# Kernel optimization log

Hardware: AMD Instinct MI355X
Metric: run time of the kernel (lower is better)

## Reference

```python
import math
import jax, jax.numpy as jnp
import numpy as np

B, N, D, H = 2, 2048, 1024, 16

def setup_inputs() -> dict:
    key = jax.random.key(0)
    ks = jax.random.split(key, 5)
    x = jax.random.normal(ks[0], (B, N, D), dtype=jnp.float32)
    # causal mask: True = masked (matches masked_fill semantics)
    mask = jnp.broadcast_to(jnp.triu(jnp.ones((N, N), dtype=bool), k=1), (B, N, N))
    sc = 0.02
    Wqkv = jax.random.normal(ks[1], (3 * D, D), dtype=jnp.float32) * sc
    bqkv = jax.random.normal(ks[2], (3 * D,), dtype=jnp.float32) * sc
    Wo = jax.random.normal(ks[3], (D, D), dtype=jnp.float32) * sc
    bo = jax.random.normal(ks[4], (D,), dtype=jnp.float32) * sc
    return {"x": x, "mask": mask, "Wqkv": Wqkv, "bqkv": bqkv, "Wo": Wo, "bo": bo}

def reference(x, mask, Wqkv, bqkv, Wo, bo):
    b, n, d = x.shape
    h = H
    s = d // h
    qkv = x @ Wqkv.T + bqkv                       # [b, n, 3d]
    q, k, v = jnp.split(qkv, 3, axis=2)           # each [b, n, d]
    def heads(z):
        return z.reshape(b, n, h, s).transpose(0, 2, 1, 3)  # [b, h, n, s]
    q, k, v = heads(q), heads(k), heads(v)
    q = q / jnp.asarray(math.sqrt(s), q.dtype)
    a = jnp.einsum('bhqs,bhks->bhqk', q, k)       # [b, h, n, n]
    a = jnp.where(mask[:, None, :, :], -jnp.inf, a)
    a = jax.nn.softmax(a, axis=-1)
    y = jnp.einsum('bhqk,bhks->bhqs', a, v)       # [b, h, n, s]
    y = y.transpose(0, 2, 1, 3).reshape(b, n, d)
    return y @ Wo.T + bo
```

## Files before the change

### kernel.cpp

```cpp
#include <hip/hip_runtime.h>
#include <hip/hip_bf16.h>
#include <stdint.h>

#define BB 2
#define NN 2048
#define DD 1024
#define HH 16
#define SS 64

typedef short short8 __attribute__((ext_vector_type(8)));
typedef float f32x4 __attribute__((ext_vector_type(4)));

__device__ __forceinline__ float bf2f(uint16_t u) {
    return __uint_as_float(((uint32_t)u) << 16);
}
__device__ __forceinline__ uint16_t f2bf(float f) {
    uint32_t u = __float_as_uint(f);
    return (uint16_t)((u + 0x7FFFu + ((u >> 16) & 1u)) >> 16);
}
__device__ __forceinline__ short8 cvt8(float4 a, float4 b) {
    short8 s;
    s[0] = (short)f2bf(a.x); s[1] = (short)f2bf(a.y);
    s[2] = (short)f2bf(a.z); s[3] = (short)f2bf(a.w);
    s[4] = (short)f2bf(b.x); s[5] = (short)f2bf(b.y);
    s[6] = (short)f2bf(b.z); s[7] = (short)f2bf(b.w);
    return s;
}

__device__ __forceinline__ void load_lds16(const uint16_t* g, uint16_t* l) {
    __builtin_amdgcn_global_load_lds(
        (const __attribute__((address_space(1))) void*)g,
        (__attribute__((address_space(3))) void*)l, 16, 0, 0);
}

#define XE  (4096 * 1024)
#define WQE (3072 * 1024)
#define WOE (1024 * 1024)

__global__ __launch_bounds__(256) void cvt_all(
    const float* __restrict__ x, const float* __restrict__ wq,
    const float* __restrict__ wo, uint16_t* __restrict__ dst)
{
    int i = (blockIdx.x * 256 + threadIdx.x) * 8;
    const float* src;
    int off;
    if (i < XE)            { src = x;  off = i; }
    else if (i < XE + WQE) { src = wq; off = i - XE; }
    else                   { src = wo; off = i - XE - WQE; }
    float4 a = *(const float4*)(src + off);
    float4 b = *(const float4*)(src + off + 4);
    *(short8*)(dst + i) = cvt8(a, b);
}

__global__ __launch_bounds__(256) void gemm_qkv(
    const uint16_t* __restrict__ X, const uint16_t* __restrict__ W,
    const float* __restrict__ bias,
    uint16_t* __restrict__ Qb, uint16_t* __restrict__ Kb, uint16_t* __restrict__ Vt)
{
    __shared__ __align__(16) uint16_t smem[18432];
    uint16_t* As0 = smem;
    uint16_t* As1 = smem + 4096;
    uint16_t* Bs0 = smem + 8192;
    uint16_t* Bs1 = smem + 12288;

    const int tid = threadIdx.x;
    const int w = tid >> 6, l = tid & 63;
    const int lq = l & 15, lg = l >> 4;
    const int wm = w >> 1, wn = w & 1;

    const int flat = blockIdx.x + blockIdx.y * 24;
    const int xcd = flat & 7, g = flat >> 3;
    const int n0 = (xcd * 3 + (g % 3)) * 128;
    const int m0 = (g / 3) * 128;

    f32x4 acc[4][4] = {};

    for (int k0 = 0; k0 < 1024; k0 += 64) {
        __syncthreads();
        #pragma unroll
        for (int j = 0; j < 2; ++j) {
            const int c = (j * 4 + w) * 64 + l;
            const size_t ra = (size_t)(m0 + (c >> 2)) * 1024 + k0 + (c & 3) * 8;
            const size_t rb = (size_t)(n0 + (c >> 2)) * 1024 + k0 + (c & 3) * 8;
            load_lds16(X + ra,      As0 + (j * 4 + w) * 512);
            load_lds16(X + ra + 32, As1 + (j * 4 + w) * 512);
            load_lds16(W + rb,      Bs0 + (j * 4 + w) * 512);
            load_lds16(W + rb + 32, Bs1 + (j * 4 + w) * 512);
        }
        __syncthreads();
        short8 af[4], bfr[4];
        #pragma unroll
        for (int mi = 0; mi < 4; ++mi)
            af[mi] = *(const short8*)&As0[(wm * 64 + mi * 16 + lq) * 32 + lg * 8];
        #pragma unroll
        for (int ni = 0; ni < 4; ++ni)
            bfr[ni] = *(const short8*)&Bs0[(wn * 64 + ni * 16 + lq) * 32 + lg * 8];
        #pragma unroll
        for (int mi = 0; mi < 4; ++mi)
            #pragma unroll
            for (int ni = 0; ni < 4; ++ni)
                acc[mi][ni] = __builtin_amdgcn_mfma_f32_16x16x32_bf16(
                    af[mi], bfr[ni], acc[mi][ni], 0, 0, 0);
        #pragma unroll
        for (int mi = 0; mi < 4; ++mi)
            af[mi] = *(const short8*)&As1[(wm * 64 + mi * 16 + lq) * 32 + lg * 8];
        #pragma unroll
        for (int ni = 0; ni < 4; ++ni)
            bfr[ni] = *(const short8*)&Bs1[(wn * 64 + ni * 16 + lq) * 32 + lg * 8];
        #pragma unroll
        for (int mi = 0; mi < 4; ++mi)
            #pragma unroll
            for (int ni = 0; ni < 4; ++ni)
                acc[mi][ni] = __builtin_amdgcn_mfma_f32_16x16x32_bf16(
                    af[mi], bfr[ni], acc[mi][ni], 0, 0, 0);
    }

    __syncthreads();
    const int part = n0 >> 10;
    const int hh = ((n0 + wn * 64) & 1023) >> 6;
    const int mrow0 = m0 + wm * 64;
    const int bh = (mrow0 >> 11) * 16 + hh;
    const int tok0 = mrow0 & 2047;
    const float scl = (part == 0) ? 0.125f * 1.44269504089f : 1.0f;

    float bias4[4];
    #pragma unroll
    for (int ni = 0; ni < 4; ++ni)
        bias4[ni] = bias[n0 + wn * 64 + ni * 16 + lq];

    uint16_t* T = smem + w * 4608;
    if (part < 2) {
        #pragma unroll
        for (int mi = 0; mi < 4; ++mi)
            #pragma unroll
            for (int ni = 0; ni < 4; ++ni)
                #pragma unroll
                for (int r = 0; r < 4; ++r)
                    T[(mi * 16 + lg * 4 + r) * 72 + ni * 16 + lq] =
                        f2bf((acc[mi][ni][r] + bias4[ni]) * scl);
    } else {
        #pragma unroll
        for (int mi = 0; mi < 4; ++mi)
            #pragma unroll
            for (int ni = 0; ni < 4; ++ni)
                #pragma unroll
                for (int r = 0; r < 4; ++r)
                    T[(ni * 16 + lq) * 72 + mi * 16 + lg * 4 + r] =
                        f2bf(acc[mi][ni][r] + bias4[ni]);
    }

    const int a0 = l >> 3, b8 = (l & 7) * 8;
    #pragma unroll
    for (int i = 0; i < 8; ++i) {
        int a = i * 8 + a0;
        short8 u = *(short8*)&T[a * 72 + b8];
        uint16_t* p;
        if (part < 2) {
            uint16_t* dst = (part == 0) ? Qb : Kb;
            p = dst + ((size_t)bh * 2048 + tok0 + a) * 64 + b8;
        } else {
            p = Vt + ((size_t)bh * 64 + a) * 2048 + tok0 + b8;
        }
        *(short8*)p = u;
    }
}

__device__ __forceinline__ void loadK8(const uint16_t* kp, short8 (&d)[8]) {
    #pragma unroll
    for (int n = 0; n < 4; ++n) {
        d[2 * n]     = *(const short8*)(kp + n * 1024);
        d[2 * n + 1] = *(const short8*)(kp + n * 1024 + 32);
    }
}
__device__ __forceinline__ void loadV8(const uint16_t* vp, short8 (&d)[8]) {
    #pragma unroll
    for (int n = 0; n < 4; ++n) {
        d[2 * n]     = *(const short8*)(vp + n * 32768);
        d[2 * n + 1] = *(const short8*)(vp + n * 32768 + 32);
    }
}

#define DEFER_THR 11.5f

__global__ __launch_bounds__(128) void attn_mfma(
    const uint16_t* __restrict__ Q, const uint16_t* __restrict__ K,
    const uint16_t* __restrict__ Vt, uint16_t* __restrict__ Y)
{
    const int id = blockIdx.x;
    const int bh = id & 31;
    const int blk = 31 - (id >> 5);
    const int qt = blk;
    const int q0 = blk * 64;

    const int wv = threadIdx.x >> 6;
    const int lane = threadIdx.x & 63;
    const int lq = lane & 15;
    const int lg = lane >> 4;

    __shared__ __align__(16) uint16_t Pl[2][2][16][72];
    __shared__ float  My[64][68];
    __shared__ float2 Mml[64];

    const uint16_t* Kb = K + (size_t)bh * (2048 * 64);
    const uint16_t* Vb = Vt + (size_t)bh * (64 * 2048);
    const int b = bh >> 4, h = bh & 15;

    short8 qf[4][2];
    #pragma unroll
    for (int sub = 0; sub < 4; ++sub) {
        const uint16_t* qb = Q + ((size_t)bh * 2048 + q0 + sub * 16 + lq) * 64 + lg * 8;
        qf[sub][0] = *(const short8*)qb;
        qf[sub][1] = *(const short8*)(qb + 32);
    }

    f32x4 y[4][4] = {};
    float m[4]    = {-INFINITY, -INFINITY, -INFINITY, -INFINITY};
    float lsum[4] = {0.f, 0.f, 0.f, 0.f};

    const uint16_t* kp = Kb + ((size_t)(wv * 64 + lq)) * 64 + lg * 8;
    const uint16_t* vp = Vb + (size_t)lq * 2048 + wv * 64 + lg * 8;

    short8 kf[8], vv[8];

    auto qkpair = [&](f32x4 (&z)[2][4], int s0) {
        __builtin_amdgcn_s_setprio(1);
        #pragma unroll
        for (int p = 0; p < 2; ++p)
            #pragma unroll
            for (int n = 0; n < 4; ++n) {
                f32x4 t = {};
                t = __builtin_amdgcn_mfma_f32_16x16x32_bf16(kf[2 * n], qf[s0 + p][0], t, 0, 0, 0);
                z[p][n] = __builtin_amdgcn_mfma_f32_16x16x32_bf16(kf[2 * n + 1], qf[s0 + p][1], t, 0, 0, 0);
            }
        __builtin_amdgcn_s_setprio(0);
    };

    auto smpv = [&](f32x4 (&z)[2][4], int s0, int kv0, bool domask) {
        if (domask) {
            #pragma unroll
            for (int p = 0; p < 2; ++p) {
                const int qrow = q0 + (s0 + p) * 16 + lq;
                #pragma unroll
                for (int n = 0; n < 4; ++n) {
                    const int kvb = kv0 + n * 16 + lg * 4;
                    #pragma unroll
                    for (int r = 0; r < 4; ++r)
                        if (kvb + r > qrow) z[p][n][r] = -INFINITY;
                }
            }
        }
        float mt[2];
        #pragma unroll
        for (int p = 0; p < 2; ++p) {
            float t = -INFINITY;
            #pragma unroll
            for (int n = 0; n < 4; ++n)
                #pragma unroll
                for (int r = 0; r < 4; ++r)
                    t = fmaxf(t, z[p][n][r]);
            mt[p] = t;
        }
        const float g = fmaxf(mt[0] - m[s0], mt[1] - m[s0 + 1]);
        const bool skip = __all(g <= DEFER_THR);
        if (!skip) {
            #pragma unroll
            for (int p = 0; p < 2; ++p) {
                const int s = s0 + p;
                float mf = fmaxf(mt[p], __shfl_xor(mt[p], 16));
                mf = fmaxf(mf, __shfl_xor(mf, 32));
                const float mn = fmaxf(m[s], mf);
                const float sc = exp2f(m[s] - mn);
                m[s] = mn;
                lsum[s] *= sc;
                float scy[4];
                #pragma unroll
                for (int r = 0; r < 4; ++r) scy[r] = __shfl(sc, lg * 4 + r);
                #pragma unroll
                for (int n = 0; n < 4; ++n)
                    #pragma unroll
                    for (int r = 0; r < 4; ++r)
                        y[s][n][r] *= scy[r];
            }
        }
        float ps[2] = {0.f, 0.f};
        #pragma unroll
        for (int p = 0; p < 2; ++p) {
            const int s = s0 + p;
            #pragma unroll
            for (int n = 0; n < 4; ++n) {
                float e0 = exp2f(z[p][n][0] - m[s]);
                float e1 = exp2f(z[p][n][1] - m[s]);
                float e2 = exp2f(z[p][n][2] - m[s]);
                float e3 = exp2f(z[p][n][3] - m[s]);
                ps[p] += (e0 + e1) + (e2 + e3);
                uint32_t p0, p1;
                asm("v_cvt_pk_bf16_f32 %0, %1, %2" : "=v"(p0) : "v"(e0), "v"(e1));
                asm("v_cvt_pk_bf16_f32 %0, %1, %2" : "=v"(p1) : "v"(e2), "v"(e3));
                uint2 u; u.x = p0; u.y = p1;
                *(uint2*)&Pl[wv][p][lq][n * 16 + lg * 4] = u;
            }
        }
        lsum[s0] += ps[0];
        lsum[s0 + 1] += ps[1];

        short8 pa[2][2];
        #pragma unroll
        for (int p = 0; p < 2; ++p) {
            pa[p][0] = *(short8*)&Pl[wv][p][lq][lg * 8];
            pa[p][1] = *(short8*)&Pl[wv][p][lq][lg * 8 + 32];
        }
        __builtin_amdgcn_s_setprio(1);
        #pragma unroll
        for (int p = 0; p < 2; ++p) {
            const int s = s0 + p;
            #pragma unroll
            for (int n = 0; n < 4; ++n) {
                y[s][n] = __builtin_amdgcn_mfma_f32_16x16x32_bf16(pa[p][0], vv[2 * n], y[s][n], 0, 0, 0);
                y[s][n] = __builtin_amdgcn_mfma_f32_16x16x32_bf16(pa[p][1], vv[2 * n + 1], y[s][n], 0, 0, 0);
            }
        }
        __builtin_amdgcn_s_setprio(0);
    };

    if (wv <= qt) {
        loadK8(kp, kf);
        int kt = wv;
        while (true) {
            const bool last = (kt + 2 > qt);
            const bool domask = (kt == qt);
            const int kv0 = kt * 64;
            loadV8(vp, vv);
            f32x4 z[2][4];
            qkpair(z, 0);
            smpv(z, 0, kv0, domask);
            qkpair(z, 2);
            if (!last) loadK8(kp + 8192, kf);
            smpv(z, 2, kv0, domask);
            if (last) break;
            kp += 8192; vp += 128; kt += 2;
        }
    }

    float ls[4];
    #pragma unroll
    for (int s = 0; s < 4; ++s) {
        float t = lsum[s];
        t += __shfl_xor(t, 16);
        t += __shfl_xor(t, 32);
        ls[s] = t;
    }

    if (wv == 1) {
        #pragma unroll
        for (int s = 0; s < 4; ++s) {
            #pragma unroll
            for (int n = 0; n < 4; ++n)
                #pragma unroll
                for (int r = 0; r < 4; ++r)
                    My[s * 16 + lg * 4 + r][n * 16 + lq] = y[s][n][r];
            if (lg == 0) Mml[s * 16 + lq] = make_float2(m[s], ls[s]);
        }
    }
    __syncthreads();
    if (wv == 0) {
        #pragma unroll
        for (int s = 0; s < 4; ++s) {
            float2 o = Mml[s * 16 + lq];
            const float m1 = o.x, l1 = o.y;
            const float mx = fmaxf(m[s], m1);
            const float w0 = exp2f(m[s] - mx);
            const float w1 = exp2f(m1 - mx);
            const float inv = 1.0f / (ls[s] * w0 + l1 * w1);
            const float f0 = w0 * inv, f1 = w1 * inv;
            float f0r[4], f1r[4];
            #pragma unroll
            for (int r = 0; r < 4; ++r) {
                f0r[r] = __shfl(f0, lg * 4 + r);
                f1r[r] = __shfl(f1, lg * 4 + r);
            }
            #pragma unroll
            for (int r = 0; r < 4; ++r) {
                int token = b * 2048 + q0 + s * 16 + lg * 4 + r;
                uint16_t* yrow = Y + (size_t)token * 1024 + h * 64;
                #pragma unroll
                for (int n = 0; n < 4; ++n) {
                    float val = y[s][n][r] * f0r[r] +
                                My[s * 16 + lg * 4 + r][n * 16 + lq] * f1r[r];
                    yrow[n * 16 + lq] = f2bf(val);
                }
            }
        }
    }
}

__global__ __launch_bounds__(256) void gemm_proj(
    const uint16_t* __restrict__ Yin, const uint16_t* __restrict__ W,
    const float* __restrict__ bias, float* __restrict__ out)
{
    __shared__ __align__(16) uint16_t smem[16384];
    uint16_t* As0 = smem;
    uint16_t* As1 = smem + 4096;
    uint16_t* Bs0 = smem + 8192;
    uint16_t* Bs1 = smem + 12288;

    const int tid = threadIdx.x;
    const int w = tid >> 6, l = tid & 63;
    const int lq = l & 15, lg = l >> 4;
    const int wm = w >> 1, wn = w & 1;

    const int flat = blockIdx.x + blockIdx.y * 8;
    const int n0 = (flat & 7) * 128;
    const int m0 = (flat >> 3) * 128;

    f32x4 acc[4][4] = {};

    for (int k0 = 0; k0 < 1024; k0 += 64) {
        __syncthreads();
        #pragma unroll
        for (int j = 0; j < 2; ++j) {
            const int c = (j * 4 + w) * 64 + l;
            const size_t ra = (size_t)(m0 + (c >> 2)) * 1024 + k0 + (c & 3) * 8;
            const size_t rb = (size_t)(n0 + (c >> 2)) * 1024 + k0 + (c & 3) * 8;
            load_lds16(Yin + ra,      As0 + (j * 4 + w) * 512);
            load_lds16(Yin + ra + 32, As1 + (j * 4 + w) * 512);
            load_lds16(W + rb,        Bs0 + (j * 4 + w) * 512);
            load_lds16(W + rb + 32,   Bs1 + (j * 4 + w) * 512);
        }
        __syncthreads();
        short8 af[4], bfr[4];
        #pragma unroll
        for (int mi = 0; mi < 4; ++mi)
            af[mi] = *(const short8*)&As0[(wm * 64 + mi * 16 + lq) * 32 + lg * 8];
        #pragma unroll
        for (int ni = 0; ni < 4; ++ni)
            bfr[ni] = *(const short8*)&Bs0[(wn * 64 + ni * 16 + lq) * 32 + lg * 8];
        #pragma unroll
        for (int mi = 0; mi < 4; ++mi)
            #pragma unroll
            for (int ni = 0; ni < 4; ++ni)
                acc[mi][ni] = __builtin_amdgcn_mfma_f32_16x16x32_bf16(
                    af[mi], bfr[ni], acc[mi][ni], 0, 0, 0);
        #pragma unroll
        for (int mi = 0; mi < 4; ++mi)
            af[mi] = *(const short8*)&As1[(wm * 64 + mi * 16 + lq) * 32 + lg * 8];
        #pragma unroll
        for (int ni = 0; ni < 4; ++ni)
            bfr[ni] = *(const short8*)&Bs1[(wn * 64 + ni * 16 + lq) * 32 + lg * 8];
        #pragma unroll
        for (int mi = 0; mi < 4; ++mi)
            #pragma unroll
            for (int ni = 0; ni < 4; ++ni)
                acc[mi][ni] = __builtin_amdgcn_mfma_f32_16x16x32_bf16(
                    af[mi], bfr[ni], acc[mi][ni], 0, 0, 0);
    }

    const int mrow0 = m0 + wm * 64;
    const int ncol0 = n0 + wn * 64;
    float bias4[4];
    #pragma unroll
    for (int ni = 0; ni < 4; ++ni)
        bias4[ni] = bias[ncol0 + ni * 16 + lq];

    #pragma unroll
    for (int mi = 0; mi < 4; ++mi)
        #pragma unroll
        for (int r = 0; r < 4; ++r) {
            const size_t rowoff = (size_t)(mrow0 + mi * 16 + lg * 4 + r) * 1024;
            #pragma unroll
            for (int ni = 0; ni < 4; ++ni)
                out[rowoff + ncol0 + ni * 16 + lq] = acc[mi][ni][r] + bias4[ni];
        }
}


extern "C" void kernel_launch(void* const* d_in, const int* in_sizes, int n_in,
                              void* d_out, int out_size, void* d_ws, size_t ws_size,
                              hipStream_t stream) {
    const float* x    = (const float*)d_in[0];
    const float* Wqkv = (const float*)d_in[2];
    const float* bqkv = (const float*)d_in[3];
    const float* Wo   = (const float*)d_in[4];
    const float* bo   = (const float*)d_in[5];

    const size_t QK = (size_t)BB * HH * NN * SS;

    uint16_t* Xb  = (uint16_t*)d_ws;
    uint16_t* Wqb = Xb + XE;
    uint16_t* Wob = Wqb + WQE;
    uint16_t* Qb  = Wob + WOE;
    uint16_t* Kb  = Qb + QK;
    uint16_t* Vt  = Kb + QK;
    uint16_t* Yb  = Vt + QK;

    cvt_all<<<(XE + WQE + WOE) / 8 / 256, 256, 0, stream>>>(x, Wqkv, Wo, Xb);
    gemm_qkv<<<dim3(24, 32), 256, 0, stream>>>(Xb, Wqb, bqkv, Qb, Kb, Vt);
    attn_mfma<<<1024, 128, 0, stream>>>(Qb, Kb, Vt, Yb);
    gemm_proj<<<dim3(8, 32), 256, 0, stream>>>(Yb, Wob, bo, (float*)d_out);
}
```

Baseline: 123.9 us.

## Split attention KV loop across four waves with tree merge of partial softmax

The attention kernel moves from two to four waves per block. Each wave processes every fourth KV tile instead of every second, and the four partial (m, l, y) states are combined with a two-level shared-memory tree merge. The goal is to shorten each block's serial KV loop and raise per-CU parallelism, most of all for late causal query tiles. In exchange it adds extra merge rounds with barriers, more LDS, and zero-sum guards for waves that got no tiles.

```diff
diff --git a/kernel.cpp b/kernel.cpp
--- a/kernel.cpp
+++ b/kernel.cpp
@@ -182,7 +182,7 @@
 
 #define DEFER_THR 11.5f
 
-__global__ __launch_bounds__(128) void attn_mfma(
+__global__ __launch_bounds__(256) void attn_mfma(
     const uint16_t* __restrict__ Q, const uint16_t* __restrict__ K,
     const uint16_t* __restrict__ Vt, uint16_t* __restrict__ Y)
 {
@@ -197,9 +197,9 @@
     const int lq = lane & 15;
     const int lg = lane >> 4;
 
-    __shared__ __align__(16) uint16_t Pl[2][2][16][72];
-    __shared__ float  My[64][68];
-    __shared__ float2 Mml[64];
+    __shared__ __align__(16) uint16_t Pl[4][2][16][72];
+    __shared__ float  Yreg[2][64][68];
+    __shared__ float2 MLreg[2][64];
 
     const uint16_t* Kb = K + (size_t)bh * (2048 * 64);
     const uint16_t* Vb = Vt + (size_t)bh * (64 * 2048);
@@ -326,7 +326,7 @@
         loadK8(kp, kf);
         int kt = wv;
         while (true) {
-            const bool last = (kt + 2 > qt);
+            const bool last = (kt + 4 > qt);
             const bool domask = (kt == qt);
             const int kv0 = kt * 64;
             loadV8(vp, vv);
@@ -334,10 +334,10 @@
             qkpair(z, 0);
             smpv(z, 0, kv0, domask);
             qkpair(z, 2);
-            if (!last) loadK8(kp + 8192, kf);
+            if (!last) loadK8(kp + 16384, kf);
             smpv(z, 2, kv0, domask);
             if (last) break;
-            kp += 8192; vp += 128; kt += 2;
+            kp += 16384; vp += 256; kt += 4;
         }
     }
 
@@ -350,44 +350,66 @@
         ls[s] = t;
     }
 
-    if (wv == 1) {
+    auto mergeFrom = [&](int reg) {
         #pragma unroll
         for (int s = 0; s < 4; ++s) {
+            float2 o = MLreg[reg][s * 16 + lq];
+            const float mo = o.x, lo = o.y;
+            const float mx = fmaxf(m[s], mo);
+            const float w0 = (ls[s] == 0.f) ? 0.f : exp2f(m[s] - mx);
+            const float w1 = (lo == 0.f) ? 0.f : exp2f(mo - mx);
+            const float ln = ls[s] * w0 + lo * w1;
+            float w0r[4], w1r[4];
+            #pragma unroll
+            for (int r = 0; r < 4; ++r) {
+                w0r[r] = __shfl(w0, lg * 4 + r);
+                w1r[r] = __shfl(w1, lg * 4 + r);
+            }
             #pragma unroll
             for (int n = 0; n < 4; ++n)
                 #pragma unroll
                 for (int r = 0; r < 4; ++r)
-                    My[s * 16 + lg * 4 + r][n * 16 + lq] = y[s][n][r];
-            if (lg == 0) Mml[s * 16 + lq] = make_float2(m[s], ls[s]);
-        }
-    }
+                    y[s][n][r] = y[s][n][r] * w0r[r] +
+                                 Yreg[reg][s * 16 + lg * 4 + r][n * 16 + lq] * w1r[r];
+            m[s] = mx;
+            ls[s] = ln;
+        }
+    };
+    auto postTo = [&](int reg) {
+        #pragma unroll
+        for (int s = 0; s < 4; ++s) {
+            #pragma unroll
+            for (int n = 0; n < 4; ++n)
+                #pragma unroll
+                for (int r = 0; r < 4; ++r)
+                    Yreg[reg][s * 16 + lg * 4 + r][n * 16 + lq] = y[s][n][r];
+            if (lg == 0) MLreg[reg][s * 16 + lq] = make_float2(m[s], ls[s]);
+        }
+    };
+
+    if (wv == 1) postTo(0);
+    if (wv == 3) postTo(1);
+    __syncthreads();
+    if (wv == 0) mergeFrom(0);
+    if (wv == 2) mergeFrom(1);
+    __syncthreads();
+    if (wv == 2) postTo(0);
     __syncthreads();
     if (wv == 0) {
+        mergeFrom(0);
         #pragma unroll
         for (int s = 0; s < 4; ++s) {
-            float2 o = Mml[s * 16 + lq];
-            const float m1 = o.x, l1 = o.y;
-            const float mx = fmaxf(m[s], m1);
-            const float w0 = exp2f(m[s] - mx);
-            const float w1 = exp2f(m1 - mx);
-            const float inv = 1.0f / (ls[s] * w0 + l1 * w1);
-            const float f0 = w0 * inv, f1 = w1 * inv;
-            float f0r[4], f1r[4];
-            #pragma unroll
-            for (int r = 0; r < 4; ++r) {
-                f0r[r] = __shfl(f0, lg * 4 + r);
-                f1r[r] = __shfl(f1, lg * 4 + r);
-            }
+            const float inv = 1.0f / ls[s];
+            float invy[4];
+            #pragma unroll
+            for (int r = 0; r < 4; ++r) invy[r] = __shfl(inv, lg * 4 + r);
             #pragma unroll
             for (int r = 0; r < 4; ++r) {
                 int token = b * 2048 + q0 + s * 16 + lg * 4 + r;
                 uint16_t* yrow = Y + (size_t)token * 1024 + h * 64;
                 #pragma unroll
-                for (int n = 0; n < 4; ++n) {
-                    float val = y[s][n][r] * f0r[r] +
-                                My[s * 16 + lg * 4 + r][n * 16 + lq] * f1r[r];
-                    yrow[n * 16 + lq] = f2bf(val);
-                }
+                for (int n = 0; n < 4; ++n)
+                    yrow[n * 16 + lq] = f2bf(y[s][n][r] * invy[r]);
             }
         }
     }
@@ -494,6 +516,6 @@
 
     cvt_all<<<(XE + WQE + WOE) / 8 / 256, 256, 0, stream>>>(x, Wqkv, Wo, Xb);
     gemm_qkv<<<dim3(24, 32), 256, 0, stream>>>(Xb, Wqb, bqkv, Qb, Kb, Vt);
-    attn_mfma<<<1024, 128, 0, stream>>>(Qb, Kb, Vt, Yb);
+    attn_mfma<<<1024, 256, 0, stream>>>(Qb, Kb, Vt, Yb);
     gemm_proj<<<dim3(8, 32), 256, 0, stream>>>(Yb, Wob, bo, (float*)d_out);
 }
```

Result: slower. 143.8 us (+16.1%).
